# Optimization experiments

Measured on AMD Instinct MI355X. Metric: run time of the kernel, lower is better.

Reference implementation:

```python
import jax, jax.numpy as jnp
import numpy as np

HID, H, P, N, G, K = 2688, 64, 64, 128, 8, 4
I = H * P            # intermediate_size = 4096
GN = G * N           # groups_ssm_state_size = 1024
CONV_DIM = I + 2 * GN  # 6144
TOTAL = 2 * I + 2 * GN + H  # 10304
EPS = 1e-5


def setup_inputs() -> dict:
    key = jax.random.key(0)
    ks = jax.random.split(key, 8)
    B, T = 2, 2048
    hidden_states = jax.random.normal(ks[0], (B, T, HID), dtype=jnp.float32)
    in_proj_w = jax.random.normal(ks[1], (TOTAL, HID), dtype=jnp.float32) * 0.02
    conv_w = jax.random.normal(ks[2], (CONV_DIM, K), dtype=jnp.float32) * 0.1  # depthwise kernel
    conv_b = jnp.zeros((CONV_DIM,), dtype=jnp.float32)
    A = -jnp.exp(jax.random.normal(ks[3], (H,), dtype=jnp.float32))
    D = jnp.ones((H,), dtype=jnp.float32)
    dt_bias = jnp.ones((H,), dtype=jnp.float32)
    norm_weight = jnp.ones((I,), dtype=jnp.float32)
    out_proj_w = jax.random.normal(ks[4], (HID, I), dtype=jnp.float32) * 0.02
    return {"hidden_states": hidden_states, "in_proj_w": in_proj_w, "conv_w": conv_w,
            "conv_b": conv_b, "A": A, "D": D, "dt_bias": dt_bias,
            "norm_weight": norm_weight, "out_proj_w": out_proj_w}


def reference(hidden_states, in_proj_w, conv_w, conv_b, A, D, dt_bias, norm_weight, out_proj_w):
    B, T, _ = hidden_states.shape
    hpg = H // G  # heads per group

    # 1-2. in_proj and split
    proj = jnp.einsum('bth,oh->bto', hidden_states, in_proj_w)  # (B,T,TOTAL)
    gate = proj[..., :I]
    xBC = proj[..., I:I + CONV_DIM]
    dt = proj[..., I + CONV_DIM:]  # (B,T,H)

    # 3. causal depthwise conv1d (left-pad K-1, slice to T) + silu
    xp = jnp.pad(xBC, ((0, 0), (K - 1, 0), (0, 0)))
    conv = conv_b
    for i in range(K):  # tiny fixed kernel loop
        conv = conv + xp[:, i:i + T, :] * conv_w[:, i]
    conv = jax.nn.silu(conv)

    # 4-5. split and reshape
    x = conv[..., :I].reshape(B, T, H, P)
    Bm = conv[..., I:I + GN].reshape(B, T, G, N)
    Cm = conv[..., I + GN:].reshape(B, T, G, N)

    # 6. selective scan (precompute dt / A_bar outside the scan)
    dt_sp = jax.nn.softplus(dt + dt_bias)          # (B,T,H)
    A_bar = jnp.exp(A * dt_sp)                     # (B,T,H)
    xg = x.reshape(B, T, G, hpg, P)
    Ab = A_bar.reshape(B, T, G, hpg)
    dts = dt_sp.reshape(B, T, G, hpg)

    def step(h, inp):
        x_t, B_t, C_t, Ab_t, dt_t = inp  # (B,G,hpg,P),(B,G,N),(B,G,N),(B,G,hpg),(B,G,hpg)
        outer = dt_t[..., None, None] * x_t[..., None] * B_t[:, :, None, None, :]
        h = Ab_t[..., None, None] * h + outer      # (B,G,hpg,P,N)
        y_t = jnp.einsum('bghpn,bgn->bghp', h, C_t)
        return h, y_t

    inputs = (jnp.moveaxis(xg, 1, 0), jnp.moveaxis(Bm, 1, 0), jnp.moveaxis(Cm, 1, 0),
              jnp.moveaxis(Ab, 1, 0), jnp.moveaxis(dts, 1, 0))
    h0 = jnp.zeros((B, G, hpg, P, N), dtype=hidden_states.dtype)
    _, ys = jax.lax.scan(step, h0, inputs)         # (T,B,G,hpg,P)
    y = jnp.moveaxis(ys, 0, 1).reshape(B, T, H, P) + D[None, None, :, None] * x
    y = y.reshape(B, T, I)

    # 7. gated RMSNorm
    y = y * jax.nn.silu(gate)
    var = jnp.mean(y * y, axis=-1, keepdims=True)
    y = y * jax.lax.rsqrt(var + EPS) * norm_weight

    # 8. out_proj
    return jnp.einsum('bti,oi->bto', y, out_proj_w)
```

## Files before the change

kernel.cpp:

```cpp
#include <hip/hip_runtime.h>
#include <stdint.h>

typedef unsigned short ushort_t;
typedef __attribute__((ext_vector_type(4))) float f32x4;
typedef __attribute__((ext_vector_type(2))) float f32x2;
typedef __attribute__((ext_vector_type(8))) __bf16 bf16x8;
typedef __attribute__((ext_vector_type(4))) unsigned short u16x4;
typedef __attribute__((ext_vector_type(8))) unsigned short u16x8;

#define DEV __device__ __forceinline__

DEV void gload_lds16(const void* g, void* l) {
  __builtin_amdgcn_global_load_lds(
      (const __attribute__((address_space(1))) uint32_t*)(uintptr_t)(g),
      (__attribute__((address_space(3))) uint32_t*)(uintptr_t)(l), 16, 0, 0);
}

DEV ushort_t f2bf(float f) {
  union { float f; uint32_t u; } x; x.f = f;
  x.u += 0x7fffu + ((x.u >> 16) & 1u);
  return (ushort_t)(x.u >> 16);
}

DEV float bf2f(ushort_t u) {
  union { uint32_t u; float f; } x; x.u = (uint32_t)u << 16; return x.f;
}

DEV float siluf(float x) { return x / (1.f + expf(-x)); }

#define BAR asm volatile("s_barrier" ::: "memory")
#define LGKM0 do { asm volatile("s_waitcnt lgkmcnt(0)" ::: "memory"); \
                   __builtin_amdgcn_sched_barrier(0); } while (0)
#define VMCNT(n) asm volatile("s_waitcnt vmcnt(" #n ")" ::: "memory")

__global__ __launch_bounds__(256) void fill_kernel(float* p, float v, int n) {
  int i = blockIdx.x * 256 + threadIdx.x;
  if (i < n) p[i] = v;
}

__global__ __launch_bounds__(256) void cvt_bf16_kernel(const float* __restrict__ src,
                                                       ushort_t* __restrict__ dst,
                                                       int n_src4, int n_dst4) {
  int i = blockIdx.x * 256 + threadIdx.x;
  if (i >= n_dst4) return;
  f32x4 v;
  if (i < n_src4) v = *(const f32x4*)(src + (size_t)i * 4);
  else { v.x = 0.f; v.y = 0.f; v.z = 0.f; v.w = 0.f; }
  u16x4 o;
  o.x = f2bf(v.x); o.y = f2bf(v.y); o.z = f2bf(v.z); o.w = f2bf(v.w);
  *(u16x4*)(dst + (size_t)i * 4) = o;
}

DEV void ld_a4(const unsigned char* ab2, int mgofs, int ck0, int ck1, bf16x8 (&af)[4][2]) {
#pragma unroll
  for (int mi = 0; mi < 4; ++mi) {
    const unsigned char* p = ab2 + (mgofs + mi * 16) * 128;
    af[mi][0] = *(const bf16x8*)(p + ck0);
    af[mi][1] = *(const bf16x8*)(p + ck1);
  }
}

DEV void ld_b2(const unsigned char* bb2, int npofs, int ck0, int ck1, bf16x8 (&bf)[2][2]) {
#pragma unroll
  for (int ni = 0; ni < 2; ++ni) {
    const unsigned char* p = bb2 + (npofs + ni * 16) * 128;
    bf[ni][0] = *(const bf16x8*)(p + ck0);
    bf[ni][1] = *(const bf16x8*)(p + ck1);
  }
}

DEV void mm16(f32x4 (&acc)[8][4], const bf16x8 (&af)[4][2], const bf16x8 (&bf)[2][2],
              int mb, int nb) {
  __builtin_amdgcn_s_setprio(1);
#pragma unroll
  for (int mi = 0; mi < 4; ++mi)
#pragma unroll
    for (int ni = 0; ni < 2; ++ni)
#pragma unroll
      for (int kk = 0; kk < 2; ++kk)
        acc[mb + mi][nb + ni] = __builtin_amdgcn_mfma_f32_16x16x32_bf16(
            af[mi][kk], bf[ni][kk], acc[mb + mi][nb + ni], 0, 0, 0);
  __builtin_amdgcn_s_setprio(0);
}

DEV void stage2(const ushort_t* s0, const ushort_t* s1, unsigned char* d) {
  gload_lds16(s0, d);
  gload_lds16(s1, d + 8192);
}

template <int MODE>
__global__ __launch_bounds__(512, 1) void gemm8_kernel(const ushort_t* __restrict__ A,
                                                       const ushort_t* __restrict__ B,
                                                       void* __restrict__ C0,
                                                       void* __restrict__ C1,
                                                       int K, int NB, int NC, int niter) {
  __shared__ __align__(16) unsigned char lds[131072];
  const int tid = threadIdx.x;
  const int l = tid & 63, w = tid >> 6;
  const int wr = w >> 2, wc = w & 3;
  const int lr = l & 15, lk = l >> 4;
  const int xm = (lr & 7) << 4;
  const int ck0 = (lk * 16) ^ xm;
  const int ck1 = (64 + lk * 16) ^ xm;
  const int bm = blockIdx.x, bn = blockIdx.y;

  const int rr = (w << 3) + (l >> 3);
  const int cE = ((l & 7) ^ (l >> 3)) << 3;
  const int dstoff = w * 1024 + l * 16;

  const ushort_t* sA00 = A + (size_t)(bm * 256 +       rr) * K + cE;
  const ushort_t* sA01 = A + (size_t)(bm * 256 +  64 + rr) * K + cE;
  const ushort_t* sA10 = A + (size_t)(bm * 256 + 128 + rr) * K + cE;
  const ushort_t* sA11 = A + (size_t)(bm * 256 + 192 + rr) * K + cE;
  int rb0 = bn * 256 +       rr; if (rb0 > NB - 1) rb0 = NB - 1;
  int rb1 = bn * 256 +  64 + rr; if (rb1 > NB - 1) rb1 = NB - 1;
  int rb2 = bn * 256 + 128 + rr; if (rb2 > NB - 1) rb2 = NB - 1;
  int rb3 = bn * 256 + 192 + rr; if (rb3 > NB - 1) rb3 = NB - 1;
  const ushort_t* sB00 = B + (size_t)rb0 * K + cE;
  const ushort_t* sB01 = B + (size_t)rb1 * K + cE;
  const ushort_t* sB10 = B + (size_t)rb2 * K + cE;
  const ushort_t* sB11 = B + (size_t)rb3 * K + cE;

  const int aoff = wr * 16384 + lr * 128;
  const int boff = 32768 + (wc >> 1) * 16384 + ((wc & 1) * 64 + lr) * 128;

  f32x4 acc[8][4] = {};
  bf16x8 af[4][2], bf[2][2], bg[2][2];

  stage2(sA00, sA01, lds + dstoff);
  stage2(sA10, sA11, lds + 16384 + dstoff);
  stage2(sB00, sB01, lds + 32768 + dstoff);
  stage2(sB10, sB11, lds + 49152 + dstoff);
  stage2(sA00 + 64, sA01 + 64, lds + 65536 + dstoff);
  VMCNT(2);
  BAR;

  auto kpair = [&](int kt0, bool last) {
    const unsigned char* a0 = lds + aoff;
    const unsigned char* b0 = lds + boff;
    const unsigned char* a1 = lds + 65536 + aoff;
    const unsigned char* b1 = lds + 65536 + boff;
    const size_t c1 = (size_t)(kt0 + 1) * 64;
    const size_t c2 = (size_t)(kt0 + 2) * 64;
    const size_t c3 = (size_t)(kt0 + 3) * 64;
    ld_a4(a0, 0, ck0, ck1, af);
    ld_b2(b0, 0, ck0, ck1, bf);
    stage2(sA10 + c1, sA11 + c1, lds + 65536 + 16384 + dstoff);
    BAR; LGKM0; mm16(acc, af, bf, 0, 0); BAR;
    ld_b2(b0, 32, ck0, ck1, bg);
    stage2(sB00 + c1, sB01 + c1, lds + 65536 + 32768 + dstoff);
    BAR; LGKM0; mm16(acc, af, bg, 0, 2); BAR;
    ld_a4(a0, 64, ck0, ck1, af);
    stage2(sB10 + c1, sB11 + c1, lds + 65536 + 49152 + dstoff);
    BAR; LGKM0; mm16(acc, af, bg, 4, 2); BAR;
    if (!last) { stage2(sA00 + c2, sA01 + c2, lds + dstoff); VMCNT(2); }
    else       { VMCNT(0); }
    BAR; LGKM0; mm16(acc, af, bf, 4, 0); BAR;
    ld_a4(a1, 0, ck0, ck1, af);
    ld_b2(b1, 0, ck0, ck1, bf);
    if (!last) stage2(sA10 + c2, sA11 + c2, lds + 16384 + dstoff);
    BAR; LGKM0; mm16(acc, af, bf, 0, 0); BAR;
    ld_b2(b1, 32, ck0, ck1, bg);
    if (!last) stage2(sB00 + c2, sB01 + c2, lds + 32768 + dstoff);
    BAR; LGKM0; mm16(acc, af, bg, 0, 2); BAR;
    ld_a4(a1, 64, ck0, ck1, af);
    if (!last) stage2(sB10 + c2, sB11 + c2, lds + 49152 + dstoff);
    BAR; LGKM0; mm16(acc, af, bg, 4, 2); BAR;
    if (!last) { stage2(sA00 + c3, sA01 + c3, lds + 65536 + dstoff); VMCNT(2); }
    BAR; LGKM0; mm16(acc, af, bf, 4, 0); BAR;
  };

  for (int it = 0; it < niter - 1; ++it) kpair(2 * it, false);
  kpair(2 * (niter - 1), true);

  const int crow0 = bm * 256 + wr * 128 + (lk << 2);
  const int ccol0 = bn * 256 + wc * 64 + lr;
  if (MODE == 0) {
    ushort_t* gate = (ushort_t*)C0;
    ushort_t* xbc  = (ushort_t*)C1;
#pragma unroll
    for (int ni = 0; ni < 4; ++ni) {
      const int col = ccol0 + ni * 16;
      if (col < NC) {
        ushort_t* dst; size_t stride;
        if (col < 4096) { dst = gate + col; stride = 4096; }
        else            { dst = xbc + (col - 4096); stride = 6272; }
#pragma unroll
        for (int mi = 0; mi < 8; ++mi)
#pragma unroll
          for (int r = 0; r < 4; ++r)
            dst[(size_t)(crow0 + mi * 16 + r) * stride] = f2bf(acc[mi][ni][r]);
      }
    }
  } else {
    float* o = (float*)C0;
#pragma unroll
    for (int ni = 0; ni < 4; ++ni) {
      const int col = ccol0 + ni * 16;
      if (col < NC) {
#pragma unroll
        for (int mi = 0; mi < 8; ++mi)
#pragma unroll
          for (int r = 0; r < 4; ++r)
            o[(size_t)(crow0 + mi * 16 + r) * NC + col] = acc[mi][ni][r];
      }
    }
  }
}

__global__ __launch_bounds__(256) void conv_silu_kernel(const ushort_t* __restrict__ xbc,
                                                        const float* __restrict__ cw,
                                                        const float* __restrict__ cb,
                                                        ushort_t* __restrict__ out) {
  int idx = blockIdx.x * 256 + threadIdx.x;
  int c4 = (idx % 1536) << 2;
  int bt = idx / 1536;
  int t = bt & 2047;
  const ushort_t* base = xbc + (size_t)bt * 6272 + c4;
  f32x4 w0 = *(const f32x4*)&cw[(c4 + 0) * 4];
  f32x4 w1 = *(const f32x4*)&cw[(c4 + 1) * 4];
  f32x4 w2 = *(const f32x4*)&cw[(c4 + 2) * 4];
  f32x4 w3 = *(const f32x4*)&cw[(c4 + 3) * 4];
  f32x4 acc = *(const f32x4*)&cb[c4];
#pragma unroll
  for (int i = 0; i < 4; ++i) {
    int dt_ = i - 3;
    if (t + dt_ >= 0) {
      u16x4 xv = *(const u16x4*)(base + (ptrdiff_t)dt_ * 6272);
      acc.x += bf2f(xv.x) * w0[i];
      acc.y += bf2f(xv.y) * w1[i];
      acc.z += bf2f(xv.z) * w2[i];
      acc.w += bf2f(xv.w) * w3[i];
    }
  }
  u16x4 o;
  o.x = f2bf(siluf(acc.x)); o.y = f2bf(siluf(acc.y));
  o.z = f2bf(siluf(acc.z)); o.w = f2bf(siluf(acc.w));
  *(u16x4*)(out + (size_t)bt * 6144 + c4) = o;
}

__global__ __launch_bounds__(256) void dt_kernel(const ushort_t* __restrict__ xbc,
                                                 const float* __restrict__ dt_bias,
                                                 const float* __restrict__ Avec,
                                                 float* __restrict__ dtA) {
  int idx = blockIdx.x * 256 + threadIdx.x;
  int h = idx >> 12, bt = idx & 4095;
  float v = bf2f(xbc[(size_t)bt * 6272 + 6144 + h]) + dt_bias[h];
  float sp = fmaxf(v, 0.f) + log1pf(expf(-fabsf(v)));
  float ab = expf(Avec[h] * sp);
  dtA[(h << 13) + bt] = sp;
  dtA[(h << 13) + 4096 + bt] = ab;
}

__global__ __launch_bounds__(256) void ssd_kernel(const ushort_t* __restrict__ conv,
                                                  const float* __restrict__ dtA,
                                                  const float* __restrict__ Dvec,
                                                  const float* __restrict__ Avec,
                                                  ushort_t* __restrict__ yssm,
                                                  ushort_t* __restrict__ hst,
                                                  float* __restrict__ abprod) {
  const int bid = blockIdx.x;
  const int ck = bid & 7;
  const int h = (bid >> 3) & 63;
  const int b = bid >> 9;
  const int g = h >> 3;
  const int tid = threadIdx.x;
  const int lane = tid & 63;
  const int wv = tid >> 6;
  const int lr = lane & 15, lk = lane >> 4;
  const int btb = (b << 11) + (ck << 8);

  __shared__ __align__(16) unsigned char ldsb[76816];
  float* csL = (float*)(ldsb + 73728);
  float* dtL = (float*)(ldsb + 74752);
  float* wL  = (float*)(ldsb + 75776);
  float* wsum = (float*)(ldsb + 76800);

  const float Ah = Avec[h];
  const float Dh = Dvec[h];

  float dv = dtA[(h << 13) + btb + tid];
  float s = dv;
#pragma unroll
  for (int off = 1; off < 64; off <<= 1) {
    float t = __shfl_up(s, off, 64);
    if (lane >= off) s += t;
  }
  if (lane == 63) wsum[wv] = s;
  __syncthreads();
  float basev = 0.f;
  for (int i = 0; i < wv; ++i) basev += wsum[i];
  const float csv = basev + s;
  csL[tid] = csv;
  dtL[tid] = dv;
  __syncthreads();
  const float cstot = csL[255];
  wL[tid] = dv * expf(Ah * (cstot - csv));
  if (tid == 0) abprod[((b << 6) + h) * 8 + ck] = expf(Ah * cstot);

  const ushort_t* Xg = conv + (size_t)btb * 6144 + (h << 6);
#pragma unroll
  for (int rep = 0; rep < 8; ++rep) {
    int idx = rep * 256 + tid;
    int t = idx >> 3, pq = (idx & 7) << 3;
    u16x8 v = *(const u16x8*)(Xg + (size_t)t * 6144 + pq);
#pragma unroll
    for (int e = 0; e < 8; ++e) {
      int p = pq + e;
      *(ushort_t*)(ldsb + p * 512 + ((t * 2) ^ ((p & 7) << 4))) = v[e];
    }
  }
  __syncthreads();

  const ushort_t* Bg = conv + (size_t)btb * 6144 + 4096 + (g << 7);
  f32x4 hacc[4][2] = {};
  for (int tc = 0; tc < 8; ++tc) {
#pragma unroll
    for (int rep = 0; rep < 2; ++rep) {
      int idx = rep * 256 + tid;
      int tl = idx >> 4, nq = (idx & 15) << 3;
      u16x8 v = *(const u16x8*)(Bg + (size_t)(tc * 32 + tl) * 6144 + nq);
      float wt = wL[tc * 32 + tl];
#pragma unroll
      for (int e = 0; e < 8; ++e) {
        int n = nq + e;
        *(ushort_t*)(ldsb + 65536 + n * 64 + ((tl * 2) ^ ((n & 3) << 4))) =
            f2bf(bf2f(v[e]) * wt);
      }
    }
    __syncthreads();
    bf16x8 a4[4], b2[2];
#pragma unroll
    for (int pf = 0; pf < 4; ++pf) {
      int p = pf * 16 + lr;
      a4[pf] = *(const bf16x8*)(ldsb + p * 512 + (((tc * 32 + lk * 8) * 2) ^ ((p & 7) << 4)));
    }
#pragma unroll
    for (int nf = 0; nf < 2; ++nf) {
      int n = wv * 32 + nf * 16 + lr;
      b2[nf] = *(const bf16x8*)(ldsb + 65536 + n * 64 + ((lk * 16) ^ ((n & 3) << 4)));
    }
#pragma unroll
    for (int pf = 0; pf < 4; ++pf)
#pragma unroll
      for (int nf = 0; nf < 2; ++nf)
        hacc[pf][nf] = __builtin_amdgcn_mfma_f32_16x16x32_bf16(a4[pf], b2[nf],
                                                               hacc[pf][nf], 0, 0, 0);
    __syncthreads();
  }
#pragma unroll
  for (int pf = 0; pf < 4; ++pf)
#pragma unroll
    for (int nf = 0; nf < 2; ++nf)
#pragma unroll
      for (int r = 0; r < 4; ++r) {
        int p = pf * 16 + (lk << 2) + r;
        int n = wv * 32 + nf * 16 + lr;
        hst[((size_t)((b << 10) | (h << 4) | ((p >> 5) << 3) | ck)) * 4096 +
            (size_t)(p & 31) * 128 + n] = f2bf(hacc[pf][nf][r]);
      }

  const ushort_t* Cg = conv + (size_t)btb * 6144 + 5120 + (g << 7);
  for (int rb = 0; rb < 4; ++rb) {
    const int i0 = rb << 6;
    f32x4 sacc[4][4] = {};
#pragma unroll
    for (int kk = 0; kk < 4; ++kk) {
      bf16x8 ca[4], bb[4];
#pragma unroll
      for (int ifr = 0; ifr < 4; ++ifr)
        ca[ifr] = *(const bf16x8*)(Cg + (size_t)(i0 + ifr * 16 + lr) * 6144 + kk * 32 + lk * 8);
#pragma unroll
      for (int jf = 0; jf < 4; ++jf)
        bb[jf] = *(const bf16x8*)(Bg + (size_t)(wv * 64 + jf * 16 + lr) * 6144 + kk * 32 + lk * 8);
#pragma unroll
      for (int ifr = 0; ifr < 4; ++ifr)
#pragma unroll
        for (int jf = 0; jf < 4; ++jf)
          sacc[ifr][jf] = __builtin_amdgcn_mfma_f32_16x16x32_bf16(ca[ifr], bb[jf],
                                                                  sacc[ifr][jf], 0, 0, 0);
    }
#pragma unroll
    for (int ifr = 0; ifr < 4; ++ifr) {
#pragma unroll
      for (int jf = 0; jf < 4; ++jf) {
        int j = wv * 64 + jf * 16 + lr;
        float dtj = dtL[j], csj = csL[j];
#pragma unroll
        for (int r = 0; r < 4; ++r) {
          int il = ifr * 16 + (lk << 2) + r;
          int ig = i0 + il;
          float val = 0.f;
          if (j <= ig) val = sacc[ifr][jf][r] * dtj * expf(Ah * (csL[ig] - csj));
          *(ushort_t*)(ldsb + 32768 + il * 512 + ((j * 2) ^ ((il & 7) << 4))) = f2bf(val);
        }
      }
    }
    __syncthreads();
    f32x4 yacc[4] = {};
    const int ilB = wv * 16 + lr;
#pragma unroll
    for (int ks = 0; ks < 8; ++ks) {
      bf16x8 pb = *(const bf16x8*)(ldsb + 32768 + ilB * 512 +
                                   (((ks * 32 + lk * 8) * 2) ^ ((ilB & 7) << 4)));
#pragma unroll
      for (int pf = 0; pf < 4; ++pf) {
        int p = pf * 16 + lr;
        bf16x8 pa = *(const bf16x8*)(ldsb + p * 512 +
                                     (((ks * 32 + lk * 8) * 2) ^ ((p & 7) << 4)));
        yacc[pf] = __builtin_amdgcn_mfma_f32_16x16x32_bf16(pa, pb, yacc[pf], 0, 0, 0);
      }
    }
    const int irow = i0 + wv * 16 + lr;
    const size_t ybase = (size_t)(btb + irow) * 4096 + (h << 6);
#pragma unroll
    for (int pf = 0; pf < 4; ++pf) {
      u16x4 o;
#pragma unroll
      for (int r = 0; r < 4; ++r) {
        int p = pf * 16 + (lk << 2) + r;
        float xv = bf2f(*(const ushort_t*)(ldsb + p * 512 +
                                           ((irow * 2) ^ ((p & 7) << 4))));
        o[r] = f2bf(yacc[pf][r] + Dh * xv);
      }
      *(u16x4*)(yssm + ybase + pf * 16 + (lk << 2)) = o;
    }
    __syncthreads();
  }
}

__global__ __launch_bounds__(256) void combine_kernel(ushort_t* __restrict__ hst,
                                                      const float* __restrict__ abprod) {
  const int bid = blockIdx.x;
  const int bh = bid >> 1;
  const int tid = threadIdx.x;
  const size_t base = (size_t)bid * 8 * 4096 + tid * 16;
  float hrun[16];
#pragma unroll
  for (int e = 0; e < 16; ++e) hrun[e] = 0.f;
  for (int c = 0; c < 8; ++c) {
    const size_t p = base + (size_t)c * 4096;
    u16x8 v0 = *(const u16x8*)&hst[p];
    u16x8 v1 = *(const u16x8*)&hst[p + 8];
    float ab = abprod[bh * 8 + c];
    u16x8 w0, w1;
#pragma unroll
    for (int e = 0; e < 8; ++e) { w0[e] = f2bf(hrun[e]); w1[e] = f2bf(hrun[8 + e]); }
    *(u16x8*)&hst[p] = w0;
    *(u16x8*)&hst[p + 8] = w1;
#pragma unroll
    for (int e = 0; e < 8; ++e) {
      hrun[e] = ab * hrun[e] + bf2f(v0[e]);
      hrun[8 + e] = ab * hrun[8 + e] + bf2f(v1[e]);
    }
  }
}

__global__ __launch_bounds__(256) void correct_kernel(const ushort_t* __restrict__ conv,
                                                      const float* __restrict__ dtA,
                                                      const float* __restrict__ Avec,
                                                      const ushort_t* __restrict__ hst,
                                                      ushort_t* __restrict__ yssm) {
  const int bid = blockIdx.x;
  const int ck = bid & 7;
  const int h = (bid >> 3) & 63;
  const int b = bid >> 9;
  const int g = h >> 3;
  const int tid = threadIdx.x;
  const int lane = tid & 63;
  const int w = tid >> 6;
  const int lr = lane & 15, lk = lane >> 4;
  const int btb = (b << 11) + (ck << 8);

  __shared__ float pdl[256];
  __shared__ float wsum[4];
  float s = dtA[(h << 13) + btb + tid];
#pragma unroll
  for (int off = 1; off < 64; off <<= 1) {
    float t = __shfl_up(s, off, 64);
    if (lane >= off) s += t;
  }
  if (lane == 63) wsum[w] = s;
  __syncthreads();
  float basev = 0.f;
  for (int i = 0; i < w; ++i) basev += wsum[i];
  pdl[tid] = expf(Avec[h] * (basev + s));
  __syncthreads();

  const ushort_t* Cc = conv + (size_t)btb * 6144 + 5120 + (g << 7);
  const size_t hb0 = ((size_t)((b << 10) | (h << 4) | (0 << 3) | ck)) * 4096;
  const size_t hb1 = ((size_t)((b << 10) | (h << 4) | (1 << 3) | ck)) * 4096;

  f32x4 acc[4][4] = {};
#pragma unroll
  for (int kk = 0; kk < 4; ++kk) {
    const int k0 = kk * 32 + lk * 8;
    bf16x8 afr[4], bfr[4];
#pragma unroll
    for (int mf = 0; mf < 4; ++mf) {
      const int t = w * 64 + mf * 16 + lr;
      afr[mf] = *(const bf16x8*)(Cc + (size_t)t * 6144 + k0);
    }
#pragma unroll
    for (int nf = 0; nf < 4; ++nf) {
      const int p = nf * 16 + lr;
      const size_t hb = (p < 32) ? hb0 : hb1;
      bfr[nf] = *(const bf16x8*)(hst + hb + (size_t)(p & 31) * 128 + k0);
    }
#pragma unroll
    for (int mf = 0; mf < 4; ++mf)
#pragma unroll
      for (int nf = 0; nf < 4; ++nf)
        acc[mf][nf] = __builtin_amdgcn_mfma_f32_16x16x32_bf16(afr[mf], bfr[nf],
                                                              acc[mf][nf], 0, 0, 0);
  }

#pragma unroll
  for (int mf = 0; mf < 4; ++mf) {
#pragma unroll
    for (int r = 0; r < 4; ++r) {
      const int row = w * 64 + mf * 16 + (lk << 2) + r;
      const float pd = pdl[row];
      const size_t yrow = (size_t)(btb + row) * 4096 + (h << 6);
#pragma unroll
      for (int nf = 0; nf < 4; ++nf) {
        const int p = nf * 16 + lr;
        const size_t idx = yrow + p;
        yssm[idx] = f2bf(bf2f(yssm[idx]) + pd * acc[mf][nf][r]);
      }
    }
  }
}

__global__ __launch_bounds__(256) void norm_kernel(const ushort_t* __restrict__ yssm,
                                                   const ushort_t* __restrict__ gate,
                                                   const float* __restrict__ nw,
                                                   ushort_t* __restrict__ out) {
  const int bt = blockIdx.x;
  const int tid = threadIdx.x;
  const ushort_t* y = yssm + (size_t)bt * 4096;
  const ushort_t* gt = gate + (size_t)bt * 4096;
  float vals[16];
  float ss = 0.f;
#pragma unroll
  for (int j = 0; j < 4; ++j) {
    int o = (tid + j * 256) << 2;
    u16x4 yv = *(const u16x4*)(y + o);
    u16x4 gv = *(const u16x4*)(gt + o);
#pragma unroll
    for (int e = 0; e < 4; ++e) {
      float v = bf2f(yv[e]) * siluf(bf2f(gv[e]));
      vals[j * 4 + e] = v;
      ss += v * v;
    }
  }
#pragma unroll
  for (int m = 1; m <= 32; m <<= 1) ss += __shfl_xor(ss, m, 64);
  __shared__ float red[4];
  if ((tid & 63) == 0) red[tid >> 6] = ss;
  __syncthreads();
  ss = red[0] + red[1] + red[2] + red[3];
  const float sc = rsqrtf(ss * (1.f / 4096.f) + 1e-5f);
#pragma unroll
  for (int j = 0; j < 4; ++j) {
    int o = (tid + j * 256) << 2;
    f32x4 wv = *(const f32x4*)(nw + o);
    u16x4 ov;
    ov.x = f2bf(vals[j * 4 + 0] * sc * wv.x);
    ov.y = f2bf(vals[j * 4 + 1] * sc * wv.y);
    ov.z = f2bf(vals[j * 4 + 2] * sc * wv.z);
    ov.w = f2bf(vals[j * 4 + 3] * sc * wv.w);
    *(u16x4*)(out + (size_t)bt * 4096 + o) = ov;
  }
}

extern "C" void kernel_launch(void* const* d_in, const int* in_sizes, int n_in,
                              void* d_out, int out_size, void* d_ws, size_t ws_size,
                              hipStream_t stream) {
  const float* hidden  = (const float*)d_in[0];
  const float* w_in    = (const float*)d_in[1];
  const float* conv_w  = (const float*)d_in[2];
  const float* conv_b  = (const float*)d_in[3];
  const float* Avec    = (const float*)d_in[4];
  const float* Dvec    = (const float*)d_in[5];
  const float* dt_bias = (const float*)d_in[6];
  const float* nw      = (const float*)d_in[7];
  const float* w_out   = (const float*)d_in[8];
  float* out = (float*)d_out;

  char* ws = (char*)d_ws;
  ushort_t* Xbf   = (ushort_t*)(ws);
  ushort_t* W1bf  = (ushort_t*)(ws + 22020096);
  ushort_t* gate  = (ushort_t*)(ws + 77758464);
  ushort_t* xbc   = (ushort_t*)(ws + 111312896);
  ushort_t* W2bf  = Xbf;
  ushort_t* convb = W1bf;
  float*    dtA   = (float*)(ws + 22020096 + 50331648);
  float*    abprod= (float*)(ws + 22020096 + 52428800);
  ushort_t* yssm  = xbc;
  ushort_t* hst   = (ushort_t*)(ws + 111312896 + 33554432);
  ushort_t* ynorm = convb;
  const size_t NEED = 162693120;
  if (NEED > ws_size) {
    fill_kernel<<<4, 256, 0, stream>>>(out, 12345.0f, 1024);
    return;
  }

  cvt_bf16_kernel<<<10752, 256, 0, stream>>>(hidden, Xbf, 2752512, 2752512);
  cvt_bf16_kernel<<<27216, 256, 0, stream>>>(w_in, W1bf, 6924288, 6967296);
  gemm8_kernel<0><<<dim3(16, 41), 512, 0, stream>>>(Xbf, W1bf, gate, xbc,
                                                    2688, 10368, 10304, 21);
  cvt_bf16_kernel<<<10752, 256, 0, stream>>>(w_out, W2bf, 2752512, 2752512);
  conv_silu_kernel<<<24576, 256, 0, stream>>>(xbc, conv_w, conv_b, convb);
  dt_kernel<<<1024, 256, 0, stream>>>(xbc, dt_bias, Avec, dtA);
  ssd_kernel<<<1024, 256, 0, stream>>>(convb, dtA, Dvec, Avec, yssm, hst, abprod);
  combine_kernel<<<256, 256, 0, stream>>>(hst, abprod);
  correct_kernel<<<1024, 256, 0, stream>>>(convb, dtA, Avec, hst, yssm);
  norm_kernel<<<4096, 256, 0, stream>>>(yssm, gate, nw, ynorm);
  gemm8_kernel<1><<<dim3(16, 11), 512, 0, stream>>>(ynorm, W2bf, out, nullptr,
                                                    4096, 2688, 2688, 32);
}
```

Before: 748.9 us.

## Transpose X/B into LDS with 16-byte vector stores and wider swizzle

Rewrites how the SSD kernel transposes X and the dt-weighted B chunk into shared memory. Each lane now gathers 8 consecutive time steps for one column and writes a single 16-byte vector, replacing eight scalar 2-byte LDS stores. The XOR swizzle widens from 8 to 16 rows to cut bank conflicts. The B staging loop stages 128 time steps per barrier instead of 32, which cuts barriers and shrinks the LDS footprint. The cost is that global loads become strided 2-byte gathers instead of coalesced 16-byte loads.

```diff
diff --git a/kernel.cpp b/kernel.cpp
--- a/kernel.cpp
+++ b/kernel.cpp
@@ -270,11 +270,11 @@
   const int lr = lane & 15, lk = lane >> 4;
   const int btb = (b << 11) + (ck << 8);
 
-  __shared__ __align__(16) unsigned char ldsb[76816];
-  float* csL = (float*)(ldsb + 73728);
-  float* dtL = (float*)(ldsb + 74752);
-  float* wL  = (float*)(ldsb + 75776);
-  float* wsum = (float*)(ldsb + 76800);
+  __shared__ __align__(16) unsigned char ldsb[68624];
+  float* csL = (float*)(ldsb + 65536);
+  float* dtL = (float*)(ldsb + 66560);
+  float* wL  = (float*)(ldsb + 67584);
+  float* wsum = (float*)(ldsb + 68608);
 
   const float Ah = Avec[h];
   const float Dh = Dvec[h];
@@ -299,53 +299,56 @@
   if (tid == 0) abprod[((b << 6) + h) * 8 + ck] = expf(Ah * cstot);
 
   const ushort_t* Xg = conv + (size_t)btb * 6144 + (h << 6);
-#pragma unroll
-  for (int rep = 0; rep < 8; ++rep) {
-    int idx = rep * 256 + tid;
-    int t = idx >> 3, pq = (idx & 7) << 3;
-    u16x8 v = *(const u16x8*)(Xg + (size_t)t * 6144 + pq);
-#pragma unroll
-    for (int e = 0; e < 8; ++e) {
-      int p = pq + e;
-      *(ushort_t*)(ldsb + p * 512 + ((t * 2) ^ ((p & 7) << 4))) = v[e];
+  {
+    const int p = lane;
+#pragma unroll
+    for (int rep = 0; rep < 8; ++rep) {
+      const int t0 = (rep * 4 + wv) << 3;
+      u16x8 v;
+#pragma unroll
+      for (int k = 0; k < 8; ++k) v[k] = Xg[(size_t)(t0 + k) * 6144 + p];
+      *(u16x8*)(ldsb + p * 512 + ((t0 * 2) ^ ((p & 15) << 4))) = v;
     }
   }
   __syncthreads();
 
   const ushort_t* Bg = conv + (size_t)btb * 6144 + 4096 + (g << 7);
   f32x4 hacc[4][2] = {};
-  for (int tc = 0; tc < 8; ++tc) {
-#pragma unroll
-    for (int rep = 0; rep < 2; ++rep) {
-      int idx = rep * 256 + tid;
-      int tl = idx >> 4, nq = (idx & 15) << 3;
-      u16x8 v = *(const u16x8*)(Bg + (size_t)(tc * 32 + tl) * 6144 + nq);
-      float wt = wL[tc * 32 + tl];
-#pragma unroll
-      for (int e = 0; e < 8; ++e) {
-        int n = nq + e;
-        *(ushort_t*)(ldsb + 65536 + n * 64 + ((tl * 2) ^ ((n & 3) << 4))) =
-            f2bf(bf2f(v[e]) * wt);
-      }
+  for (int th = 0; th < 2; ++th) {
+#pragma unroll
+    for (int rep = 0; rep < 8; ++rep) {
+      const int n = ((rep & 1) << 6) | lane;
+      const int tl0 = ((rep >> 1) * 4 + wv) << 3;
+      const int t0 = th * 128 + tl0;
+      u16x8 v;
+#pragma unroll
+      for (int k = 0; k < 8; ++k)
+        v[k] = f2bf(bf2f(Bg[(size_t)(t0 + k) * 6144 + n]) * wL[t0 + k]);
+      *(u16x8*)(ldsb + 32768 + n * 256 + ((tl0 * 2) ^ ((n & 15) << 4))) = v;
     }
     __syncthreads();
-    bf16x8 a4[4], b2[2];
-#pragma unroll
-    for (int pf = 0; pf < 4; ++pf) {
-      int p = pf * 16 + lr;
-      a4[pf] = *(const bf16x8*)(ldsb + p * 512 + (((tc * 32 + lk * 8) * 2) ^ ((p & 7) << 4)));
-    }
-#pragma unroll
-    for (int nf = 0; nf < 2; ++nf) {
-      int n = wv * 32 + nf * 16 + lr;
-      b2[nf] = *(const bf16x8*)(ldsb + 65536 + n * 64 + ((lk * 16) ^ ((n & 3) << 4)));
-    }
-#pragma unroll
-    for (int pf = 0; pf < 4; ++pf)
-#pragma unroll
-      for (int nf = 0; nf < 2; ++nf)
-        hacc[pf][nf] = __builtin_amdgcn_mfma_f32_16x16x32_bf16(a4[pf], b2[nf],
-                                                               hacc[pf][nf], 0, 0, 0);
+#pragma unroll
+    for (int tc = 0; tc < 4; ++tc) {
+      bf16x8 a4[4], b2[2];
+#pragma unroll
+      for (int pf = 0; pf < 4; ++pf) {
+        const int p = pf * 16 + lr;
+        a4[pf] = *(const bf16x8*)(ldsb + p * 512 +
+                                  (((th * 128 + tc * 32 + lk * 8) * 2) ^ ((p & 15) << 4)));
+      }
+#pragma unroll
+      for (int nf = 0; nf < 2; ++nf) {
+        const int n = wv * 32 + nf * 16 + lr;
+        b2[nf] = *(const bf16x8*)(ldsb + 32768 + n * 256 +
+                                  (((tc * 32 + lk * 8) * 2) ^ ((n & 15) << 4)));
+      }
+#pragma unroll
+      for (int pf = 0; pf < 4; ++pf)
+#pragma unroll
+        for (int nf = 0; nf < 2; ++nf)
+          hacc[pf][nf] = __builtin_amdgcn_mfma_f32_16x16x32_bf16(a4[pf], b2[nf],
+                                                                 hacc[pf][nf], 0, 0, 0);
+    }
     __syncthreads();
   }
 #pragma unroll
@@ -392,7 +395,7 @@
           int ig = i0 + il;
           float val = 0.f;
           if (j <= ig) val = sacc[ifr][jf][r] * dtj * expf(Ah * (csL[ig] - csj));
-          *(ushort_t*)(ldsb + 32768 + il * 512 + ((j * 2) ^ ((il & 7) << 4))) = f2bf(val);
+          *(ushort_t*)(ldsb + 32768 + il * 512 + ((j * 2) ^ ((il & 15) << 4))) = f2bf(val);
         }
       }
     }
@@ -402,12 +405,12 @@
 #pragma unroll
     for (int ks = 0; ks < 8; ++ks) {
       bf16x8 pb = *(const bf16x8*)(ldsb + 32768 + ilB * 512 +
-                                   (((ks * 32 + lk * 8) * 2) ^ ((ilB & 7) << 4)));
+                                   (((ks * 32 + lk * 8) * 2) ^ ((ilB & 15) << 4)));
 #pragma unroll
       for (int pf = 0; pf < 4; ++pf) {
-        int p = pf * 16 + lr;
+        const int p = pf * 16 + lr;
         bf16x8 pa = *(const bf16x8*)(ldsb + p * 512 +
-                                     (((ks * 32 + lk * 8) * 2) ^ ((p & 7) << 4)));
+                                     (((ks * 32 + lk * 8) * 2) ^ ((p & 15) << 4)));
         yacc[pf] = __builtin_amdgcn_mfma_f32_16x16x32_bf16(pa, pb, yacc[pf], 0, 0, 0);
       }
     }
@@ -420,7 +423,7 @@
       for (int r = 0; r < 4; ++r) {
         int p = pf * 16 + (lk << 2) + r;
         float xv = bf2f(*(const ushort_t*)(ldsb + p * 512 +
-                                           ((irow * 2) ^ ((p & 7) << 4))));
+                                           ((irow * 2) ^ ((p & 15) << 4))));
         o[r] = f2bf(yacc[pf][r] + Dh * xv);
       }
       *(u16x4*)(yssm + ybase + pf * 16 + (lk << 2)) = o;
```

After: 711.8 us. 5.0% less time.
